# Performance work log

Hardware: AMD Instinct MI355X
Metric: run time of the kernel (lower is better)

Reference implementation:

```python
import jax, jax.numpy as jnp
import numpy as np

V, DM, IMG, H, M = 32000, 256, 512, 256, 16
B, K, L, T = 16, 32, 32, 128

def setup_inputs():
    key = jax.random.key(0)
    ks = jax.random.split(key, 22)
    s = 0.02
    p = lambda i, shape: jax.random.normal(ks[i], shape, jnp.float32) * s
    return {
        "ctx_input_ids": jax.random.randint(ks[0], (B, K, L), 0, V),
        "ctx_attn_mask": jnp.ones((B, K, L), jnp.int32),
        "ctx_img_emb": jax.random.normal(ks[1], (B, K, IMG), jnp.float32),
        "tgt_input_ids": jax.random.randint(ks[2], (B, T), 0, V),
        "emb_text": p(3, (V, DM)),
        "Wih_t": p(4, (3 * DM, DM)), "Whh_t": p(5, (3 * DM, DM)),
        "bih_t": p(6, (3 * DM,)), "bhh_t": p(7, (3 * DM,)),
        "fuse_W": p(8, (H, DM + IMG)), "fuse_b": p(9, (H,)),
        "mem_init": p(10, (M, H)),
        "Wih_c": p(11, (3 * H, H)), "Whh_c": p(12, (3 * H, H)),
        "bih_c": p(13, (3 * H,)), "bhh_c": p(14, (3 * H,)),
        "tok_emb": p(15, (V, H)),
        "Wih_d": p(16, (3 * H, H)), "Whh_d": p(17, (3 * H, H)),
        "bih_d": p(18, (3 * H,)), "bhh_d": p(19, (3 * H,)),
        "head_W": p(20, (V, H)), "head_b": p(21, (V,)),
    }

def _gru(x, h0, Wih, Whh, bih, bhh, mask=None):
    # x: (B, S, I) -> outs (B, S, Hd), hN (B, Hd). PyTorch GRU equations.
    xg = jnp.einsum('bti,gi->btg', x, Wih) + bih  # precompute input-side gates (B,S,3H)
    if mask is None:
        mask = jnp.ones(x.shape[:2], bool)
    def step(h, inp):
        xt, mt = inp  # (B,3H), (B,)
        hg = h @ Whh.T + bhh
        xr, xz, xn = jnp.split(xt, 3, -1)
        hr, hz, hn = jnp.split(hg, 3, -1)
        r = jax.nn.sigmoid(xr + hr)
        z = jax.nn.sigmoid(xz + hz)
        n = jnp.tanh(xn + r * hn)
        h_new = (1.0 - z) * n + z * h
        h = jnp.where(mt[:, None], h_new, h)  # hold state on padded steps
        return h, h
    hN, outs = jax.lax.scan(step, h0, (jnp.moveaxis(xg, 1, 0), jnp.moveaxis(mask, 1, 0)))
    return jnp.moveaxis(outs, 0, 1), hN

def _forward(ctx_input_ids, ctx_attn_mask, ctx_img_emb, tgt_input_ids,
             emb_text, Wih_t, Whh_t, bih_t, bhh_t, fuse_W, fuse_b, mem_init,
             Wih_c, Whh_c, bih_c, bhh_c, tok_emb, Wih_d, Whh_d, bih_d, bhh_d,
             head_W, head_b):
    b, k, l = ctx_input_ids.shape
    dm = emb_text.shape[1]
    h = fuse_W.shape[0]
    # FrameTextEncoder: embedding + masked GRU, final hidden per frame
    tok = emb_text[ctx_input_ids.reshape(b * k, l)]  # (BK, L, DM)
    mask = ctx_attn_mask.reshape(b * k, l).astype(bool)
    _, tvec = _gru(tok, jnp.zeros((b * k, dm), tok.dtype), Wih_t, Whh_t, bih_t, bhh_t, mask)
    tvec = tvec.reshape(b, k, dm)
    # Fuse text + image
    z = jnp.tanh(jnp.concatenate([tvec, ctx_img_emb], -1) @ fuse_W.T + fuse_b)  # (B,K,H)
    # Memory slot loop over K frames (sequential softmax read then erase/add write)
    mem0 = jnp.broadcast_to(mem_init, (b,) + mem_init.shape)
    inv_sqrt_d = 1.0 / float(np.sqrt(h))
    def mem_step(mem, q):
        w = jax.nn.softmax(jnp.einsum('bmd,bd->bm', mem, q) * inv_sqrt_d, -1)
        readout = jnp.einsum('bm,bmd->bd', w, mem)
        mem = mem * (1.0 - w[..., None]) + w[..., None] * q[:, None, :]
        return mem, q + readout
    _, z_mem = jax.lax.scan(mem_step, mem0, jnp.moveaxis(z, 1, 0))
    z2 = jnp.moveaxis(z_mem, 0, 1)  # (B, K, H)
    _, h0 = _gru(z2, jnp.zeros((b, h), z2.dtype), Wih_c, Whh_c, bih_c, bhh_c)
    # Decoder over target tokens (teacher forcing)
    x = tok_emb[tgt_input_ids[:, :-1]]  # (B, T-1, H)
    outs, _ = _gru(x, h0, Wih_d, Whh_d, bih_d, bhh_d)
    return outs @ head_W.T + head_b  # (B, T-1, V)

def reference(ctx_input_ids, ctx_attn_mask, ctx_img_emb, tgt_input_ids,
              emb_text, Wih_t, Whh_t, bih_t, bhh_t, fuse_W, fuse_b, mem_init,
              Wih_c, Whh_c, bih_c, bhh_c, tok_emb, Wih_d, Whh_d, bih_d, bhh_d,
              head_W, head_b):
    return _forward(ctx_input_ids, ctx_attn_mask, ctx_img_emb, tgt_input_ids,
                    emb_text, Wih_t, Whh_t, bih_t, bhh_t, fuse_W, fuse_b, mem_init,
                    Wih_c, Whh_c, bih_c, bhh_c, tok_emb, Wih_d, Whh_d, bih_d, bhh_d,
                    head_W, head_b)
```

## Files before the change

kernel.cpp:

```cpp
#include <hip/hip_runtime.h>
#include <hip/hip_bf16.h>

typedef __attribute__((ext_vector_type(4))) float f32x4;
typedef __attribute__((ext_vector_type(8))) short short8;
typedef __attribute__((ext_vector_type(4))) unsigned int u32x4;
typedef __attribute__((ext_vector_type(4))) unsigned short u16x4;

static __device__ __forceinline__ unsigned short f2bf(float f){
  unsigned u = __builtin_bit_cast(unsigned, f);
  u += 0x7FFFu + ((u >> 16) & 1u);
  return (unsigned short)(u >> 16);
}
static __device__ __forceinline__ float bf2f(unsigned short b){
  return __builtin_bit_cast(float, ((unsigned)b) << 16);
}
static __device__ __forceinline__ unsigned char f2e4m3(float x){
  unsigned u = __builtin_bit_cast(unsigned, x);
  unsigned s = (u >> 24) & 0x80u;
  float ax = __builtin_fabsf(x);
  if (ax < 0.015625f) {
    int q = (int)(ax * 512.f + 0.5f);
    return (unsigned char)(s | (unsigned)q);
  }
  if (ax > 448.f) return (unsigned char)(s | 0x7Eu);
  unsigned v = __builtin_bit_cast(unsigned, ax);
  v += 0x00080000u + ((v >> 20) & 1u);
  if (__builtin_bit_cast(float, v & 0xFFF00000u) > 448.f)
    return (unsigned char)(s | 0x7Eu);
  unsigned ee = ((v >> 23) & 0xFFu) - 127u + 7u;
  unsigned m = (v >> 20) & 7u;
  return (unsigned char)(s | (ee << 3) | m);
}
static __device__ __forceinline__ unsigned char h2fp8(float hx16){
#if __has_builtin(__builtin_amdgcn_cvt_pk_fp8_f32)
  int pk = __builtin_amdgcn_cvt_pk_fp8_f32(hx16, hx16, 0, false);
  return (unsigned char)(pk & 0xFF);
#else
  return f2e4m3(hx16);
#endif
}
static __device__ __forceinline__ f32x4 mfma16(short8 a, short8 b, f32x4 c){
  return __builtin_amdgcn_mfma_f32_16x16x32_bf16(a, b, c, 0, 0, 0);
}
static __device__ __forceinline__ f32x4 mfma8(long a, long b, f32x4 c){
  return __builtin_amdgcn_mfma_f32_16x16x32_fp8_fp8(a, b, c, 0, 0, 0);
}
static __device__ __forceinline__ float rcpf(float x){ return __builtin_amdgcn_rcpf(x); }
static __device__ __forceinline__ float sigf(float x){ return rcpf(1.f + __expf(-x)); }
static __device__ __forceinline__ float tanhfast(float x){
  float e = __expf(2.f*x);
  return (e - 1.f) * rcpf(e + 1.f);
}
static __device__ __forceinline__ float spread4(f32x4 v, int l15, int l4){
  float x0 = __shfl(v[0], l15, 64);
  float x1 = __shfl(v[1], l15, 64);
  float x2 = __shfl(v[2], l15, 64);
  float x3 = __shfl(v[3], l15, 64);
  float s01 = (l4 & 1) ? x1 : x0;
  float s23 = (l4 & 1) ? x3 : x2;
  return (l4 & 2) ? s23 : s01;
}

__global__ __launch_bounds__(256) void k_cvt(
    const float* __restrict__ sh, unsigned short* __restrict__ dh,
    const float* __restrict__ s0, const float* __restrict__ s1,
    const float* __restrict__ s2, const float* __restrict__ s3,
    const float* __restrict__ s4, const float* __restrict__ s5,
    const float* __restrict__ s6,
    unsigned short* __restrict__ d0, unsigned short* __restrict__ d1,
    unsigned short* __restrict__ d2, unsigned short* __restrict__ d3,
    unsigned short* __restrict__ d4, unsigned short* __restrict__ d5,
    unsigned short* __restrict__ d6)
{
  const long NH4 = 2048000;
  const long NS4 = 49152;
  const long total = NH4 + 7*NS4;
  for (long idx = (long)blockIdx.x*blockDim.x + threadIdx.x; idx < total;
       idx += (long)gridDim.x*blockDim.x) {
    const float* s; unsigned short* d; long off;
    if (idx < NH4) { s = sh; d = dh; off = idx; }
    else {
      long r = idx - NH4; int mat = (int)(r / NS4); off = r - (long)mat*NS4;
      switch (mat) {
        case 0: s=s0; d=d0; break;  case 1: s=s1; d=d1; break;
        case 2: s=s2; d=d2; break;  case 3: s=s3; d=d3; break;
        case 4: s=s4; d=d4; break;  case 5: s=s5; d=d5; break;
        default: s=s6; d=d6; break;
      }
    }
    f32x4 v = ((const f32x4*)s)[off];
    u16x4 o2;
    o2[0]=f2bf(v[0]); o2[1]=f2bf(v[1]); o2[2]=f2bf(v[2]); o2[3]=f2bf(v[3]);
    ((u16x4*)d)[off] = o2;
  }
}

__global__ __launch_bounds__(256) void k_cvtw(
    const float* __restrict__ s0, const float* __restrict__ s1,
    const float* __restrict__ s2,
    unsigned short* __restrict__ r0, unsigned short* __restrict__ r1,
    unsigned short* __restrict__ r2,
    unsigned char* __restrict__ z0, unsigned char* __restrict__ z1,
    unsigned char* __restrict__ z2)
{
  int idx = blockIdx.x*256 + threadIdx.x;
  if (idx >= 3*24576) return;
  int mat = idx / 24576, c = idx % 24576;
  const float* s = (mat==0) ? s0 : (mat==1 ? s1 : s2);
  if (c < 8192) {
    unsigned short* d = (mat==0) ? r0 : (mat==1 ? r1 : r2);
    int w = c >> 9, rest = c & 511;
    int kb = rest >> 6, lane = rest & 63;
    int row = w*16 + (lane & 15);
    int k0  = kb*32 + (lane >> 4)*8;
    const float* sp = s + (long)row*256 + k0;
    f32x4 a = *(const f32x4*)sp;
    f32x4 b = *(const f32x4*)(sp + 4);
    short8 o;
    o[0]=(short)f2bf(a[0]); o[1]=(short)f2bf(a[1]);
    o[2]=(short)f2bf(a[2]); o[3]=(short)f2bf(a[3]);
    o[4]=(short)f2bf(b[0]); o[5]=(short)f2bf(b[1]);
    o[6]=(short)f2bf(b[2]); o[7]=(short)f2bf(b[3]);
    *(short8*)(d + (long)c*8) = o;
  } else {
    int c2 = c - 8192;
    unsigned char* d = (mat==0) ? z0 : (mat==1 ? z1 : z2);
    int w = c2 >> 10, rest = c2 & 1023;
    int g = rest >> 9, r_ = rest & 511;
    int kb = r_ >> 6, lane = r_ & 63;
    int row = (1+g)*256 + w*16 + (lane & 15);
    int k0  = kb*32 + (lane >> 4)*8;
    const float* sp = s + (long)row*256 + k0;
    f32x4 a = *(const f32x4*)sp;
    f32x4 b = *(const f32x4*)(sp + 4);
    unsigned char ob[8];
    ob[0]=f2e4m3(a[0]*16.f); ob[1]=f2e4m3(a[1]*16.f);
    ob[2]=f2e4m3(a[2]*16.f); ob[3]=f2e4m3(a[3]*16.f);
    ob[4]=f2e4m3(b[0]*16.f); ob[5]=f2e4m3(b[1]*16.f);
    ob[6]=f2e4m3(b[2]*16.f); ob[7]=f2e4m3(b[3]*16.f);
    unsigned lo = (unsigned)ob[0] | ((unsigned)ob[1]<<8) |
                  ((unsigned)ob[2]<<16) | ((unsigned)ob[3]<<24);
    unsigned hi = (unsigned)ob[4] | ((unsigned)ob[5]<<8) |
                  ((unsigned)ob[6]<<16) | ((unsigned)ob[7]<<24);
    *(unsigned*)(d + (long)c2*8)     = lo;
    *(unsigned*)(d + (long)c2*8 + 4) = hi;
  }
}

template<int TN, int TS, int EPI>
__global__ __launch_bounds__(256) void k_gemm(
    const float* __restrict__ tabA, int ldA,
    const float* __restrict__ tabB2, int ldB2, int K1,
    const int* __restrict__ ids,
    const unsigned short* __restrict__ W,
    const float* __restrict__ bias,
    int M, int Ktot,
    void* __restrict__ outp, int ldOut)
{
  const int bm = blockIdx.x, bn = blockIdx.y;
  const int tid = threadIdx.x;
  const int lane = tid & 63, w = tid >> 6;
  const int l15 = lane & 15, l4 = lane >> 4;

  const int r_g = bm*64 + w*16 + l15;
  const int r_c = (r_g < M) ? r_g : (M-1);
  long row_src;
  if (ids) { int ii = (r_c / TN) * TS + (r_c % TN); row_src = ids[ii]; }
  else row_src = r_c;

  const int kchunk = l4 * 8;
  const int ncol0 = bn*128 + l15;

  f32x4 acc[8];
  #pragma unroll
  for (int i=0;i<8;i++){ f32x4 z4 = {0.f,0.f,0.f,0.f}; acc[i]=z4; }

  const int KB = Ktot >> 5;
  for (int kb = 0; kb < KB; ++kb) {
    int k = kb*32 + kchunk;
    const float* ap;
    if (tabB2 && k >= K1) ap = tabB2 + row_src*(long)ldB2 + (k - K1);
    else                  ap = tabA  + row_src*(long)ldA  + k;
    f32x4 a0 = *(const f32x4*)ap;
    f32x4 a1 = *(const f32x4*)(ap + 4);
    short8 afr;
    afr[0]=(short)f2bf(a0[0]); afr[1]=(short)f2bf(a0[1]);
    afr[2]=(short)f2bf(a0[2]); afr[3]=(short)f2bf(a0[3]);
    afr[4]=(short)f2bf(a1[0]); afr[5]=(short)f2bf(a1[1]);
    afr[6]=(short)f2bf(a1[2]); afr[7]=(short)f2bf(a1[3]);
    #pragma unroll
    for (int ct=0; ct<8; ++ct) {
      int n = ncol0 + ct*16;
      short8 bfr = *(const short8*)(W + (long)n*Ktot + k);
      acc[ct] = mfma16(afr, bfr, acc[ct]);
    }
  }

  #pragma unroll
  for (int ct=0; ct<8; ++ct) {
    int n = ncol0 + ct*16;
    float bv = bias[n];
    #pragma unroll
    for (int q=0; q<4; ++q) {
      int rr = bm*64 + w*16 + l4*4 + q;
      if (rr < M) {
        float v = acc[ct][q] + bv;
        if (EPI == 1) ((float*)outp)[(long)rr*ldOut + n] = tanhfast(v);
        else ((unsigned short*)outp)[(long)rr*ldOut + n] = f2bf(v);
      }
    }
  }
}

__global__ __launch_bounds__(1024, 1) void k_gru(
    const unsigned short* __restrict__ WR,
    const unsigned char*  __restrict__ WZN,
    const float* __restrict__ bhh,
    const unsigned short* __restrict__ xg,
    const int* __restrict__ mask,
    const unsigned short* __restrict__ h0bf,
    float* __restrict__ hNf,
    unsigned short* __restrict__ hNbf,
    unsigned short* __restrict__ outs,
    int T)
{
  __shared__ unsigned short hbz[9*264];
  __shared__ unsigned char  h8z[9*264];

  const int tid = threadIdx.x;
  const int w = tid >> 6, lane = tid & 63;
  const int l15 = lane & 15, l4 = lane >> 4;
  const int rowbase = blockIdx.x * 4;
  const int u = w*16 + l15;
  const int gr = l4;

  short8 Br[8];
  long Bz8[8], Bn8[8];
  #pragma unroll
  for (int kb=0; kb<8; ++kb) {
    Br[kb]  = *(const short8*)(WR + ((long)(w*8+kb)*512) + lane*8);
    Bz8[kb] = *(const long*)(WZN + ((long)((w*2+0)*8+kb)*512) + lane*8);
    Bn8[kb] = *(const long*)(WZN + ((long)((w*2+1)*8+kb)*512) + lane*8);
  }

  const float b_r = bhh[u], b_z = bhh[256+u], b_n = bhh[512+u];

  const int arow0 = (l15 < 4) ? l15     : 8;
  const int arow1 = (l15 < 4) ? 4 + l15 : 8;
  const int hbO0 = (arow0*264 + l4*8)*2;
  const int hbO1 = (arow1*264 + l4*8)*2;
  const int h8O0 =  arow0*264 + l4*8;
  const int h8O1 =  arow1*264 + l4*8;

  if (tid < 264) { hbz[8*264 + tid] = 0; h8z[8*264 + tid] = 0; }
  float h = h0bf ? bf2f(h0bf[(rowbase+gr)*256 + u]) : 0.f;
  hbz[gr*264 + u] = f2bf(h);
  h8z[gr*264 + u] = h2fp8(h * 16.f);
  __syncthreads();

  const float inv256 = 0.00390625f;

  for (int t=0; t<T; ++t) {
    const int p = t & 1;

    const long xrow = (long)(rowbase + gr)*T + t;
    const unsigned short* xp = xg + xrow*768;
    const unsigned short xr_ = xp[u];
    const unsigned short xz_ = xp[256+u];
    const unsigned short xn_ = xp[512+u];
    const int mok = mask ? mask[xrow] : 1;

    const int hbO = p ? hbO1 : hbO0;
    const int h8O = p ? h8O1 : h8O0;
    f32x4 aR={0.f,0.f,0.f,0.f}, aZ={0.f,0.f,0.f,0.f}, aN={0.f,0.f,0.f,0.f};
    #pragma unroll
    for (int kb=0; kb<8; ++kb) {
      short8 af = *(const short8*)((const char*)hbz + hbO + kb*64);
      long   a8 = *(const long*)((const char*)h8z + h8O + kb*32);
      aR = mfma16(af, Br[kb], aR);
      aZ = mfma8(a8, Bz8[kb], aZ);
      aN = mfma8(a8, Bn8[kb], aN);
    }

    float gR = spread4(aR, l15, l4);
    float gZ = spread4(aZ, l15, l4);
    float gN = spread4(aN, l15, l4);

    float rr = sigf(bf2f(xr_) + gR + b_r);
    float zz = sigf(bf2f(xz_) + gZ*inv256 + b_z);
    float nn = tanhfast(bf2f(xn_) + rr*(gN*inv256 + b_n));
    float hv = nn + zz*(h - nn);
    if (!mok) hv = h;
    h = hv;
    const int wrow = (p^1)*4 + gr;
    const unsigned short hbv = f2bf(hv);
    hbz[wrow*264 + u] = hbv;
    h8z[wrow*264 + u] = h2fp8(hv * 16.f);
    if (outs) outs[xrow*256 + u] = hbv;
    __syncthreads();
  }

  if (hNf)  hNf[(long)(rowbase+gr)*256 + u] = h;
  if (hNbf) hNbf[(rowbase+gr)*256 + u] = f2bf(h);
}

__global__ __launch_bounds__(64) void k_mem(
    const float* __restrict__ z,
    const float* __restrict__ mem_init,
    float* __restrict__ z2)
{
  const int b = blockIdx.x;
  const int lane = threadIdx.x;
  float mem[16][4];
  #pragma unroll
  for (int m=0; m<16; ++m) {
    f32x4 v = *(const f32x4*)(mem_init + m*256 + lane*4);
    mem[m][0]=v[0]; mem[m][1]=v[1]; mem[m][2]=v[2]; mem[m][3]=v[3];
  }
  for (int t=0; t<32; ++t) {
    f32x4 q = *(const f32x4*)(z + ((long)b*32 + t)*256 + lane*4);
    float s[16];
    #pragma unroll
    for (int m=0; m<16; ++m)
      s[m] = mem[m][0]*q[0] + mem[m][1]*q[1] + mem[m][2]*q[2] + mem[m][3]*q[3];
    #pragma unroll
    for (int st=1; st<64; st<<=1) {
      #pragma unroll
      for (int m=0; m<16; ++m) s[m] += __shfl_xor(s[m], st, 64);
    }
    float mx = -1e30f;
    #pragma unroll
    for (int m=0; m<16; ++m) { s[m] *= 0.0625f; mx = fmaxf(mx, s[m]); }
    float sum = 0.f;
    #pragma unroll
    for (int m=0; m<16; ++m) { s[m] = __expf(s[m]-mx); sum += s[m]; }
    float inv = rcpf(sum);
    f32x4 ro = {0.f,0.f,0.f,0.f};
    #pragma unroll
    for (int m=0; m<16; ++m) {
      float wm = s[m]*inv;
      #pragma unroll
      for (int c=0; c<4; ++c) {
        ro[c] += wm * mem[m][c];
        mem[m][c] += wm * (q[c] - mem[m][c]);
      }
    }
    f32x4 o = q + ro;
    *(f32x4*)(z2 + ((long)b*32 + t)*256 + lane*4) = o;
  }
}

__global__ __launch_bounds__(256) void k_head(
    const unsigned short* __restrict__ A,
    const unsigned short* __restrict__ Bw,
    const float* __restrict__ bias,
    float* __restrict__ out,
    int M)
{
  __shared__ unsigned short Bs[32768];
  const int bid = blockIdx.x;
  const int mt = bid % 16, nt = bid / 16;
  const int tid = threadIdx.x;
  const int lane = tid & 63, w = tid >> 6;
  const int l15 = lane & 15, l4 = lane >> 4;

  const long nbase = (long)nt * 128;
  #pragma unroll
  for (int it=0; it<16; ++it) {
    int idx = it*256 + tid;
    int rr = idx >> 5;
    int ch = idx & 31;
    int sch = ch ^ (rr & 7);
    u32x4 v = *(const u32x4*)(Bw + (nbase+rr)*256 + sch*8);
    *(u32x4*)&Bs[(long)idx*8] = v;
  }
  __syncthreads();

  const int m0 = mt*128 + w*32;
  const int arow0 = m0 + l15, arow1 = arow0 + 16;
  const int kc = l4 * 8;

  f32x4 acc[2][8];
  #pragma unroll
  for (int rt=0; rt<2; ++rt)
    #pragma unroll
    for (int ct=0; ct<8; ++ct){ f32x4 z4={0.f,0.f,0.f,0.f}; acc[rt][ct]=z4; }

  #pragma unroll
  for (int kb=0; kb<8; ++kb) {
    short8 a0 = *(const short8*)(A + (long)arow0*256 + kb*32 + kc);
    short8 a1 = *(const short8*)(A + (long)arow1*256 + kb*32 + kc);
    int c = kb*4 + l4;
    #pragma unroll
    for (int ct=0; ct<8; ++ct) {
      int n_local = ct*16 + l15;
      int sc = c ^ (n_local & 7);
      short8 bf = *(const short8*)&Bs[((long)n_local*32 + sc)*8];
      acc[0][ct] = mfma16(a0, bf, acc[0][ct]);
      acc[1][ct] = mfma16(a1, bf, acc[1][ct]);
    }
  }

  #pragma unroll
  for (int ct=0; ct<8; ++ct) {
    int n_g = nt*128 + ct*16 + l15;
    float bv = bias[n_g];
    #pragma unroll
    for (int rt=0; rt<2; ++rt) {
      #pragma unroll
      for (int q=0; q<4; ++q) {
        int r_g = m0 + rt*16 + l4*4 + q;
        if (r_g < M) out[(long)r_g*32000 + n_g] = acc[rt][ct][q] + bv;
      }
    }
  }
}

extern "C" void kernel_launch(void* const* d_in, const int* in_sizes, int n_in,
                              void* d_out, int out_size, void* d_ws, size_t ws_size,
                              hipStream_t stream)
{
  (void)in_sizes; (void)n_in; (void)out_size; (void)ws_size;
  const int*   ctx_ids  = (const int*)  d_in[0];
  const int*   ctx_mask = (const int*)  d_in[1];
  const float* img      = (const float*)d_in[2];
  const int*   tgt_ids  = (const int*)  d_in[3];
  const float* emb_text = (const float*)d_in[4];
  const float* Wih_t    = (const float*)d_in[5];
  const float* Whh_t    = (const float*)d_in[6];
  const float* bih_t    = (const float*)d_in[7];
  const float* bhh_t    = (const float*)d_in[8];
  const float* fuse_W   = (const float*)d_in[9];
  const float* fuse_b   = (const float*)d_in[10];
  const float* mem_init = (const float*)d_in[11];
  const float* Wih_c    = (const float*)d_in[12];
  const float* Whh_c    = (const float*)d_in[13];
  const float* bih_c    = (const float*)d_in[14];
  const float* bhh_c    = (const float*)d_in[15];
  const float* tok_emb  = (const float*)d_in[16];
  const float* Wih_d    = (const float*)d_in[17];
  const float* Whh_d    = (const float*)d_in[18];
  const float* bih_d    = (const float*)d_in[19];
  const float* bhh_d    = (const float*)d_in[20];
  const float* head_W   = (const float*)d_in[21];
  const float* head_b   = (const float*)d_in[22];
  float* out = (float*)d_out;
  char* ws = (char*)d_ws;

  size_t o = 0;
  auto alloc = [&](size_t bytes){ size_t r = o; o += (bytes + 255) & ~(size_t)255; return r; };
  unsigned short* wWih_t = (unsigned short*)(ws + alloc(768*256*2));
  unsigned short* wWhh_t = (unsigned short*)(ws + alloc(768*256*2));
  unsigned short* wWih_c = (unsigned short*)(ws + alloc(768*256*2));
  unsigned short* wWhh_c = (unsigned short*)(ws + alloc(768*256*2));
  unsigned short* wWih_d = (unsigned short*)(ws + alloc(768*256*2));
  unsigned short* wWhh_d = (unsigned short*)(ws + alloc(768*256*2));
  unsigned short* wFuse  = (unsigned short*)(ws + alloc(256*768*2));
  unsigned short* wR_t   = (unsigned short*)(ws + alloc(65536*2));
  unsigned short* wR_c   = (unsigned short*)(ws + alloc(65536*2));
  unsigned short* wR_d   = (unsigned short*)(ws + alloc(65536*2));
  unsigned char*  wZN_t  = (unsigned char*)(ws + alloc(131072));
  unsigned char*  wZN_c  = (unsigned char*)(ws + alloc(131072));
  unsigned char*  wZN_d  = (unsigned char*)(ws + alloc(131072));
  unsigned short* wHead  = (unsigned short*)(ws + alloc((size_t)32000*256*2));
  unsigned short* xg_t   = (unsigned short*)(ws + alloc((size_t)16384*768*2));
  unsigned short* xg_c   = (unsigned short*)(ws + alloc((size_t)512*768*2));
  unsigned short* xg_d   = (unsigned short*)(ws + alloc((size_t)2032*768*2));
  float*          tvec   = (float*)(ws + alloc((size_t)512*256*4));
  float*          zbuf   = (float*)(ws + alloc((size_t)512*256*4));
  float*          z2buf  = (float*)(ws + alloc((size_t)512*256*4));
  unsigned short* outsb  = (unsigned short*)(ws + alloc((size_t)2048*256*2));
  unsigned short* hbdec  = (unsigned short*)(ws + alloc((size_t)16*256*2));

  k_cvt<<<2048, 256, 0, stream>>>(head_W, wHead,
      Wih_t, Whh_t, Wih_c, Whh_c, Wih_d, Whh_d, fuse_W,
      wWih_t, wWhh_t, wWih_c, wWhh_c, wWih_d, wWhh_d, wFuse);
  k_cvtw<<<288, 256, 0, stream>>>(Whh_t, Whh_c, Whh_d,
                                  wR_t, wR_c, wR_d, wZN_t, wZN_c, wZN_d);

  k_gemm<32,32,0><<<dim3(256,6), 256, 0, stream>>>(
      emb_text, 256, nullptr, 0, 256, ctx_ids, wWih_t, bih_t, 16384, 256, xg_t, 768);

  k_gemm<127,128,0><<<dim3(32,6), 256, 0, stream>>>(
      tok_emb, 256, nullptr, 0, 256, tgt_ids, wWih_d, bih_d, 2032, 256, xg_d, 768);

  k_gru<<<128, 1024, 0, stream>>>(wR_t, wZN_t, bhh_t, xg_t, ctx_mask,
                                  nullptr, tvec, nullptr, nullptr, 32);

  k_gemm<1,1,1><<<dim3(8,2), 256, 0, stream>>>(
      tvec, 256, img, 512, 256, nullptr, wFuse, fuse_b, 512, 768, zbuf, 256);

  k_mem<<<16, 64, 0, stream>>>(zbuf, mem_init, z2buf);

  k_gemm<1,1,0><<<dim3(8,6), 256, 0, stream>>>(
      z2buf, 256, nullptr, 0, 256, nullptr, wWih_c, bih_c, 512, 256, xg_c, 768);

  k_gru<<<4, 1024, 0, stream>>>(wR_c, wZN_c, bhh_c, xg_c, nullptr,
                                nullptr, nullptr, hbdec, nullptr, 32);

  k_gru<<<4, 1024, 0, stream>>>(wR_d, wZN_d, bhh_d, xg_d, nullptr,
                                hbdec, nullptr, nullptr, outsb, 127);

  k_head<<<4000, 256, 0, stream>>>(outsb, wHead, head_b, out, 2032);
}
```

Before: 670.8 us.

## Run all GRU recurrent gates in FP8 and pre-convert embedding tables to bf16

The recurrent r-gate matmul in the GRU kernel now uses FP8 MFMA like the z and n gates, with a single packed FP8 weight layout. This drops the bf16 hidden-state shared buffer and the bf16 weight registers, shortening the serial per-step work. Separately, both full embedding tables are converted to bf16 up front so the input-projection GEMMs can load bf16 A fragments directly. The trade-offs are lower precision on the r gate and a large extra pass that reads and writes the full 32000-row tables on every call.

Result: faster. 655.7 us (-2.3%).

```diff
diff --git a/kernel.cpp b/kernel.cpp
--- a/kernel.cpp
+++ b/kernel.cpp
@@ -63,29 +63,27 @@
 
 __global__ __launch_bounds__(256) void k_cvt(
     const float* __restrict__ sh, unsigned short* __restrict__ dh,
+    const float* __restrict__ se, unsigned short* __restrict__ de,
+    const float* __restrict__ st, unsigned short* __restrict__ dt,
     const float* __restrict__ s0, const float* __restrict__ s1,
     const float* __restrict__ s2, const float* __restrict__ s3,
-    const float* __restrict__ s4, const float* __restrict__ s5,
-    const float* __restrict__ s6,
     unsigned short* __restrict__ d0, unsigned short* __restrict__ d1,
-    unsigned short* __restrict__ d2, unsigned short* __restrict__ d3,
-    unsigned short* __restrict__ d4, unsigned short* __restrict__ d5,
-    unsigned short* __restrict__ d6)
+    unsigned short* __restrict__ d2, unsigned short* __restrict__ d3)
 {
   const long NH4 = 2048000;
   const long NS4 = 49152;
-  const long total = NH4 + 7*NS4;
+  const long total = 3*NH4 + 4*NS4;
   for (long idx = (long)blockIdx.x*blockDim.x + threadIdx.x; idx < total;
        idx += (long)gridDim.x*blockDim.x) {
     const float* s; unsigned short* d; long off;
-    if (idx < NH4) { s = sh; d = dh; off = idx; }
+    if (idx < NH4)        { s = sh; d = dh; off = idx; }
+    else if (idx < 2*NH4) { s = se; d = de; off = idx - NH4; }
+    else if (idx < 3*NH4) { s = st; d = dt; off = idx - 2*NH4; }
     else {
-      long r = idx - NH4; int mat = (int)(r / NS4); off = r - (long)mat*NS4;
+      long r = idx - 3*NH4; int mat = (int)(r / NS4); off = r - (long)mat*NS4;
       switch (mat) {
         case 0: s=s0; d=d0; break;  case 1: s=s1; d=d1; break;
-        case 2: s=s2; d=d2; break;  case 3: s=s3; d=d3; break;
-        case 4: s=s4; d=d4; break;  case 5: s=s5; d=d5; break;
-        default: s=s6; d=d6; break;
+        case 2: s=s2; d=d2; break;  default: s=s3; d=d3; break;
       }
     }
     f32x4 v = ((const f32x4*)s)[off];
@@ -98,8 +96,6 @@
 __global__ __launch_bounds__(256) void k_cvtw(
     const float* __restrict__ s0, const float* __restrict__ s1,
     const float* __restrict__ s2,
-    unsigned short* __restrict__ r0, unsigned short* __restrict__ r1,
-    unsigned short* __restrict__ r2,
     unsigned char* __restrict__ z0, unsigned char* __restrict__ z1,
     unsigned char* __restrict__ z2)
 {
@@ -107,49 +103,33 @@
   if (idx >= 3*24576) return;
   int mat = idx / 24576, c = idx % 24576;
   const float* s = (mat==0) ? s0 : (mat==1 ? s1 : s2);
-  if (c < 8192) {
-    unsigned short* d = (mat==0) ? r0 : (mat==1 ? r1 : r2);
-    int w = c >> 9, rest = c & 511;
-    int kb = rest >> 6, lane = rest & 63;
-    int row = w*16 + (lane & 15);
-    int k0  = kb*32 + (lane >> 4)*8;
-    const float* sp = s + (long)row*256 + k0;
-    f32x4 a = *(const f32x4*)sp;
-    f32x4 b = *(const f32x4*)(sp + 4);
-    short8 o;
-    o[0]=(short)f2bf(a[0]); o[1]=(short)f2bf(a[1]);
-    o[2]=(short)f2bf(a[2]); o[3]=(short)f2bf(a[3]);
-    o[4]=(short)f2bf(b[0]); o[5]=(short)f2bf(b[1]);
-    o[6]=(short)f2bf(b[2]); o[7]=(short)f2bf(b[3]);
-    *(short8*)(d + (long)c*8) = o;
-  } else {
-    int c2 = c - 8192;
-    unsigned char* d = (mat==0) ? z0 : (mat==1 ? z1 : z2);
-    int w = c2 >> 10, rest = c2 & 1023;
-    int g = rest >> 9, r_ = rest & 511;
-    int kb = r_ >> 6, lane = r_ & 63;
-    int row = (1+g)*256 + w*16 + (lane & 15);
-    int k0  = kb*32 + (lane >> 4)*8;
-    const float* sp = s + (long)row*256 + k0;
-    f32x4 a = *(const f32x4*)sp;
-    f32x4 b = *(const f32x4*)(sp + 4);
-    unsigned char ob[8];
-    ob[0]=f2e4m3(a[0]*16.f); ob[1]=f2e4m3(a[1]*16.f);
-    ob[2]=f2e4m3(a[2]*16.f); ob[3]=f2e4m3(a[3]*16.f);
-    ob[4]=f2e4m3(b[0]*16.f); ob[5]=f2e4m3(b[1]*16.f);
-    ob[6]=f2e4m3(b[2]*16.f); ob[7]=f2e4m3(b[3]*16.f);
-    unsigned lo = (unsigned)ob[0] | ((unsigned)ob[1]<<8) |
-                  ((unsigned)ob[2]<<16) | ((unsigned)ob[3]<<24);
-    unsigned hi = (unsigned)ob[4] | ((unsigned)ob[5]<<8) |
-                  ((unsigned)ob[6]<<16) | ((unsigned)ob[7]<<24);
-    *(unsigned*)(d + (long)c2*8)     = lo;
-    *(unsigned*)(d + (long)c2*8 + 4) = hi;
-  }
-}
-
-template<int TN, int TS, int EPI>
+  unsigned char* d = (mat==0) ? z0 : (mat==1 ? z1 : z2);
+  int lane = c & 63;
+  int rest = c >> 6;
+  int kb = rest & 7;
+  int wg = rest >> 3;
+  int g = wg % 3, w = wg / 3;
+  int row = g*256 + w*16 + (lane & 15);
+  int k0  = kb*32 + (lane >> 4)*8;
+  const float* sp = s + (long)row*256 + k0;
+  f32x4 a = *(const f32x4*)sp;
+  f32x4 b = *(const f32x4*)(sp + 4);
+  unsigned char ob[8];
+  ob[0]=f2e4m3(a[0]*16.f); ob[1]=f2e4m3(a[1]*16.f);
+  ob[2]=f2e4m3(a[2]*16.f); ob[3]=f2e4m3(a[3]*16.f);
+  ob[4]=f2e4m3(b[0]*16.f); ob[5]=f2e4m3(b[1]*16.f);
+  ob[6]=f2e4m3(b[2]*16.f); ob[7]=f2e4m3(b[3]*16.f);
+  unsigned lo = (unsigned)ob[0] | ((unsigned)ob[1]<<8) |
+                ((unsigned)ob[2]<<16) | ((unsigned)ob[3]<<24);
+  unsigned hi = (unsigned)ob[4] | ((unsigned)ob[5]<<8) |
+                ((unsigned)ob[6]<<16) | ((unsigned)ob[7]<<24);
+  *(unsigned*)(d + (long)c*8)     = lo;
+  *(unsigned*)(d + (long)c*8 + 4) = hi;
+}
+
+template<int TN, int TS, int EPI, int AT>
 __global__ __launch_bounds__(256) void k_gemm(
-    const float* __restrict__ tabA, int ldA,
+    const void* __restrict__ tabA_, int ldA,
     const float* __restrict__ tabB2, int ldB2, int K1,
     const int* __restrict__ ids,
     const unsigned short* __restrict__ W,
@@ -178,16 +158,20 @@
   const int KB = Ktot >> 5;
   for (int kb = 0; kb < KB; ++kb) {
     int k = kb*32 + kchunk;
-    const float* ap;
-    if (tabB2 && k >= K1) ap = tabB2 + row_src*(long)ldB2 + (k - K1);
-    else                  ap = tabA  + row_src*(long)ldA  + k;
-    f32x4 a0 = *(const f32x4*)ap;
-    f32x4 a1 = *(const f32x4*)(ap + 4);
     short8 afr;
-    afr[0]=(short)f2bf(a0[0]); afr[1]=(short)f2bf(a0[1]);
-    afr[2]=(short)f2bf(a0[2]); afr[3]=(short)f2bf(a0[3]);
-    afr[4]=(short)f2bf(a1[0]); afr[5]=(short)f2bf(a1[1]);
-    afr[6]=(short)f2bf(a1[2]); afr[7]=(short)f2bf(a1[3]);
+    if (AT == 1) {
+      afr = *(const short8*)((const unsigned short*)tabA_ + row_src*(long)ldA + k);
+    } else {
+      const float* ap;
+      if (tabB2 && k >= K1) ap = tabB2 + row_src*(long)ldB2 + (k - K1);
+      else                  ap = (const float*)tabA_ + row_src*(long)ldA + k;
+      f32x4 a0 = *(const f32x4*)ap;
+      f32x4 a1 = *(const f32x4*)(ap + 4);
+      afr[0]=(short)f2bf(a0[0]); afr[1]=(short)f2bf(a0[1]);
+      afr[2]=(short)f2bf(a0[2]); afr[3]=(short)f2bf(a0[3]);
+      afr[4]=(short)f2bf(a1[0]); afr[5]=(short)f2bf(a1[1]);
+      afr[6]=(short)f2bf(a1[2]); afr[7]=(short)f2bf(a1[3]);
+    }
     #pragma unroll
     for (int ct=0; ct<8; ++ct) {
       int n = ncol0 + ct*16;
@@ -213,8 +197,7 @@
 }
 
 __global__ __launch_bounds__(1024, 1) void k_gru(
-    const unsigned short* __restrict__ WR,
-    const unsigned char*  __restrict__ WZN,
+    const unsigned char*  __restrict__ WF8,
     const float* __restrict__ bhh,
     const unsigned short* __restrict__ xg,
     const int* __restrict__ mask,
@@ -224,8 +207,7 @@
     unsigned short* __restrict__ outs,
     int T)
 {
-  __shared__ unsigned short hbz[9*264];
-  __shared__ unsigned char  h8z[9*264];
+  __shared__ unsigned char h8z[9*264];
 
   const int tid = threadIdx.x;
   const int w = tid >> 6, lane = tid & 63;
@@ -234,27 +216,22 @@
   const int u = w*16 + l15;
   const int gr = l4;
 
-  short8 Br[8];
-  long Bz8[8], Bn8[8];
-  #pragma unroll
-  for (int kb=0; kb<8; ++kb) {
-    Br[kb]  = *(const short8*)(WR + ((long)(w*8+kb)*512) + lane*8);
-    Bz8[kb] = *(const long*)(WZN + ((long)((w*2+0)*8+kb)*512) + lane*8);
-    Bn8[kb] = *(const long*)(WZN + ((long)((w*2+1)*8+kb)*512) + lane*8);
-  }
+  long Bf8[3][8];
+  #pragma unroll
+  for (int g=0; g<3; ++g)
+    #pragma unroll
+    for (int kb=0; kb<8; ++kb)
+      Bf8[g][kb] = *(const long*)(WF8 + ((long)((w*3+g)*8+kb)*512) + lane*8);
 
   const float b_r = bhh[u], b_z = bhh[256+u], b_n = bhh[512+u];
 
   const int arow0 = (l15 < 4) ? l15     : 8;
   const int arow1 = (l15 < 4) ? 4 + l15 : 8;
-  const int hbO0 = (arow0*264 + l4*8)*2;
-  const int hbO1 = (arow1*264 + l4*8)*2;
-  const int h8O0 =  arow0*264 + l4*8;
-  const int h8O1 =  arow1*264 + l4*8;
-
-  if (tid < 264) { hbz[8*264 + tid] = 0; h8z[8*264 + tid] = 0; }
+  const int h8O0 = arow0*264 + l4*8;
+  const int h8O1 = arow1*264 + l4*8;
+
+  if (tid < 264) h8z[8*264 + tid] = 0;
   float h = h0bf ? bf2f(h0bf[(rowbase+gr)*256 + u]) : 0.f;
-  hbz[gr*264 + u] = f2bf(h);
   h8z[gr*264 + u] = h2fp8(h * 16.f);
   __syncthreads();
 
@@ -270,33 +247,29 @@
     const unsigned short xn_ = xp[512+u];
     const int mok = mask ? mask[xrow] : 1;
 
-    const int hbO = p ? hbO1 : hbO0;
     const int h8O = p ? h8O1 : h8O0;
     f32x4 aR={0.f,0.f,0.f,0.f}, aZ={0.f,0.f,0.f,0.f}, aN={0.f,0.f,0.f,0.f};
     #pragma unroll
     for (int kb=0; kb<8; ++kb) {
-      short8 af = *(const short8*)((const char*)hbz + hbO + kb*64);
-      long   a8 = *(const long*)((const char*)h8z + h8O + kb*32);
-      aR = mfma16(af, Br[kb], aR);
-      aZ = mfma8(a8, Bz8[kb], aZ);
-      aN = mfma8(a8, Bn8[kb], aN);
-    }
-
-    float gR = spread4(aR, l15, l4);
-    float gZ = spread4(aZ, l15, l4);
-    float gN = spread4(aN, l15, l4);
+      long a8 = *(const long*)&h8z[h8O + kb*32];
+      aR = mfma8(a8, Bf8[0][kb], aR);
+      aZ = mfma8(a8, Bf8[1][kb], aZ);
+      aN = mfma8(a8, Bf8[2][kb], aN);
+    }
+
+    float gR = spread4(aR, l15, l4) * inv256;
+    float gZ = spread4(aZ, l15, l4) * inv256;
+    float gN = spread4(aN, l15, l4) * inv256;
 
     float rr = sigf(bf2f(xr_) + gR + b_r);
-    float zz = sigf(bf2f(xz_) + gZ*inv256 + b_z);
-    float nn = tanhfast(bf2f(xn_) + rr*(gN*inv256 + b_n));
+    float zz = sigf(bf2f(xz_) + gZ + b_z);
+    float nn = tanhfast(bf2f(xn_) + rr*(gN + b_n));
     float hv = nn + zz*(h - nn);
     if (!mok) hv = h;
     h = hv;
     const int wrow = (p^1)*4 + gr;
-    const unsigned short hbv = f2bf(hv);
-    hbz[wrow*264 + u] = hbv;
     h8z[wrow*264 + u] = h2fp8(hv * 16.f);
-    if (outs) outs[xrow*256 + u] = hbv;
+    if (outs) outs[xrow*256 + u] = f2bf(hv);
     __syncthreads();
   }
 
@@ -450,19 +423,15 @@
   size_t o = 0;
   auto alloc = [&](size_t bytes){ size_t r = o; o += (bytes + 255) & ~(size_t)255; return r; };
   unsigned short* wWih_t = (unsigned short*)(ws + alloc(768*256*2));
-  unsigned short* wWhh_t = (unsigned short*)(ws + alloc(768*256*2));
   unsigned short* wWih_c = (unsigned short*)(ws + alloc(768*256*2));
-  unsigned short* wWhh_c = (unsigned short*)(ws + alloc(768*256*2));
   unsigned short* wWih_d = (unsigned short*)(ws + alloc(768*256*2));
-  unsigned short* wWhh_d = (unsigned short*)(ws + alloc(768*256*2));
   unsigned short* wFuse  = (unsigned short*)(ws + alloc(256*768*2));
-  unsigned short* wR_t   = (unsigned short*)(ws + alloc(65536*2));
-  unsigned short* wR_c   = (unsigned short*)(ws + alloc(65536*2));
-  unsigned short* wR_d   = (unsigned short*)(ws + alloc(65536*2));
-  unsigned char*  wZN_t  = (unsigned char*)(ws + alloc(131072));
-  unsigned char*  wZN_c  = (unsigned char*)(ws + alloc(131072));
-  unsigned char*  wZN_d  = (unsigned char*)(ws + alloc(131072));
+  unsigned char*  wF8_t  = (unsigned char*)(ws + alloc(196608));
+  unsigned char*  wF8_c  = (unsigned char*)(ws + alloc(196608));
+  unsigned char*  wF8_d  = (unsigned char*)(ws + alloc(196608));
   unsigned short* wHead  = (unsigned short*)(ws + alloc((size_t)32000*256*2));
+  unsigned short* ebf    = (unsigned short*)(ws + alloc((size_t)32000*256*2));
+  unsigned short* tbf    = (unsigned short*)(ws + alloc((size_t)32000*256*2));
   unsigned short* xg_t   = (unsigned short*)(ws + alloc((size_t)16384*768*2));
   unsigned short* xg_c   = (unsigned short*)(ws + alloc((size_t)512*768*2));
   unsigned short* xg_d   = (unsigned short*)(ws + alloc((size_t)2032*768*2));
@@ -472,33 +441,32 @@
   unsigned short* outsb  = (unsigned short*)(ws + alloc((size_t)2048*256*2));
   unsigned short* hbdec  = (unsigned short*)(ws + alloc((size_t)16*256*2));
 
-  k_cvt<<<2048, 256, 0, stream>>>(head_W, wHead,
-      Wih_t, Whh_t, Wih_c, Whh_c, Wih_d, Whh_d, fuse_W,
-      wWih_t, wWhh_t, wWih_c, wWhh_c, wWih_d, wWhh_d, wFuse);
-  k_cvtw<<<288, 256, 0, stream>>>(Whh_t, Whh_c, Whh_d,
-                                  wR_t, wR_c, wR_d, wZN_t, wZN_c, wZN_d);
-
-  k_gemm<32,32,0><<<dim3(256,6), 256, 0, stream>>>(
-      emb_text, 256, nullptr, 0, 256, ctx_ids, wWih_t, bih_t, 16384, 256, xg_t, 768);
-
-  k_gemm<127,128,0><<<dim3(32,6), 256, 0, stream>>>(
-      tok_emb, 256, nullptr, 0, 256, tgt_ids, wWih_d, bih_d, 2032, 256, xg_d, 768);
-
-  k_gru<<<128, 1024, 0, stream>>>(wR_t, wZN_t, bhh_t, xg_t, ctx_mask,
+  k_cvt<<<4096, 256, 0, stream>>>(head_W, wHead, emb_text, ebf, tok_emb, tbf,
+      Wih_t, Wih_c, Wih_d, fuse_W,
+      wWih_t, wWih_c, wWih_d, wFuse);
+  k_cvtw<<<288, 256, 0, stream>>>(Whh_t, Whh_c, Whh_d, wF8_t, wF8_c, wF8_d);
+
+  k_gemm<32,32,0,1><<<dim3(256,6), 256, 0, stream>>>(
+      ebf, 256, nullptr, 0, 256, ctx_ids, wWih_t, bih_t, 16384, 256, xg_t, 768);
+
+  k_gemm<127,128,0,1><<<dim3(32,6), 256, 0, stream>>>(
+      tbf, 256, nullptr, 0, 256, tgt_ids, wWih_d, bih_d, 2032, 256, xg_d, 768);
+
+  k_gru<<<128, 1024, 0, stream>>>(wF8_t, bhh_t, xg_t, ctx_mask,
                                   nullptr, tvec, nullptr, nullptr, 32);
 
-  k_gemm<1,1,1><<<dim3(8,2), 256, 0, stream>>>(
+  k_gemm<1,1,1,0><<<dim3(8,2), 256, 0, stream>>>(
       tvec, 256, img, 512, 256, nullptr, wFuse, fuse_b, 512, 768, zbuf, 256);
 
   k_mem<<<16, 64, 0, stream>>>(zbuf, mem_init, z2buf);
 
-  k_gemm<1,1,0><<<dim3(8,6), 256, 0, stream>>>(
+  k_gemm<1,1,0,0><<<dim3(8,6), 256, 0, stream>>>(
       z2buf, 256, nullptr, 0, 256, nullptr, wWih_c, bih_c, 512, 256, xg_c, 768);
 
-  k_gru<<<4, 1024, 0, stream>>>(wR_c, wZN_c, bhh_c, xg_c, nullptr,
+  k_gru<<<4, 1024, 0, stream>>>(wF8_c, bhh_c, xg_c, nullptr,
                                 nullptr, nullptr, hbdec, nullptr, 32);
 
-  k_gru<<<4, 1024, 0, stream>>>(wR_d, wZN_d, bhh_d, xg_d, nullptr,
+  k_gru<<<4, 1024, 0, stream>>>(wF8_d, bhh_d, xg_d, nullptr,
                                 hbdec, nullptr, nullptr, outsb, 127);
 
   k_head<<<4000, 256, 0, stream>>>(outsb, wHead, head_b, out, 2032);
```
